# Performance work log

Hardware: AMD Instinct MI355X
Metric: run time of the kernel (lower is better)

Reference implementation:

```python
import jax, jax.numpy as jnp
import numpy as np
import math

N_USER = 100000
N_GAME = 50000
E = 200000
D = 256          # in_dim == out_dim
H = 8            # num_heads
SCALE = math.sqrt(D // H)  # sqrt(head_dim) = sqrt(32)


def setup_inputs() -> dict:
    key = jax.random.key(0)
    keys = jax.random.split(key, 64)
    it = iter(range(64))
    def nk():
        return keys[next(it)]
    s = 1.0 / math.sqrt(D)
    inp = {}
    inp["x_user"] = jax.random.normal(nk(), (N_USER, D), dtype=jnp.float32)
    inp["x_game"] = jax.random.normal(nk(), (N_GAME, D), dtype=jnp.float32)
    # node-type projections (k/q/v/out) for user and game
    for nt in ("user", "game"):
        for p in ("k", "q", "v", "out"):
            inp[f"W{p}_{nt}"] = jax.random.normal(nk(), (D, D), dtype=jnp.float32) * s
            inp[f"b{p}_{nt}"] = jax.random.normal(nk(), (D,), dtype=jnp.float32) * 0.01
    # edge-type attention + message transforms
    for et in ("played", "rev"):
        inp[f"Wa_{et}"] = jax.random.normal(nk(), (D, H), dtype=jnp.float32) * s
        inp[f"ba_{et}"] = jax.random.normal(nk(), (H,), dtype=jnp.float32) * 0.01
        inp[f"Wm_{et}"] = jax.random.normal(nk(), (D, D), dtype=jnp.float32) * s
        inp[f"bm_{et}"] = jax.random.normal(nk(), (D,), dtype=jnp.float32) * 0.01
    # edge indices: played (user -> game), rev_played (game -> user)
    inp["ei_played_src"] = jax.random.randint(nk(), (E,), 0, N_USER, dtype=jnp.int32)
    inp["ei_played_dst"] = jax.random.randint(nk(), (E,), 0, N_GAME, dtype=jnp.int32)
    inp["ei_rev_src"] = jax.random.randint(nk(), (E,), 0, N_GAME, dtype=jnp.int32)
    inp["ei_rev_dst"] = jax.random.randint(nk(), (E,), 0, N_USER, dtype=jnp.int32)
    return inp


def _lin(x, W, b):
    return x @ W + b


def _edge_pass(k_src_all, q_dst_all, v_src_all, Wa, ba, Wm, bm, src, dst, n_dst):
    # gather per-edge K/Q/V                                   [E, D]
    k_src = k_src_all[src]
    q_dst = q_dst_all[dst]
    v_src = v_src_all[src]
    # attention score MLP over head dim                       [E, H]
    scores = ((k_src * q_dst) @ Wa + ba) / SCALE
    attn = jax.nn.softmax(scores, axis=-1)  # softmax over heads (as in source)
    # message MLP                                             [E, D]
    msgs = v_src @ Wm + bm
    weighted = msgs * attn.mean(axis=-1, keepdims=True)
    # scatter-add to destination nodes
    agg = jax.ops.segment_sum(weighted, dst, num_segments=n_dst)
    cnt = jax.ops.segment_sum(jnp.ones((dst.shape[0], 1), weighted.dtype), dst, num_segments=n_dst)
    return agg, cnt


def reference(x_user, x_game,
              Wk_user, bk_user, Wq_user, bq_user, Wv_user, bv_user, Wout_user, bout_user,
              Wk_game, bk_game, Wq_game, bq_game, Wv_game, bv_game, Wout_game, bout_game,
              Wa_played, ba_played, Wm_played, bm_played,
              Wa_rev, ba_rev, Wm_rev, bm_rev,
              ei_played_src, ei_played_dst, ei_rev_src, ei_rev_dst):
    # per-node-type K/Q/V projections
    k_u = _lin(x_user, Wk_user, bk_user)
    q_u = _lin(x_user, Wq_user, bq_user)
    v_u = _lin(x_user, Wv_user, bv_user)
    k_g = _lin(x_game, Wk_game, bk_game)
    q_g = _lin(x_game, Wq_game, bq_game)
    v_g = _lin(x_game, Wv_game, bv_game)

    # user --played--> game
    agg_game, cnt_game = _edge_pass(k_u, q_g, v_u, Wa_played, ba_played, Wm_played, bm_played,
                                    ei_played_src, ei_played_dst, N_GAME)
    # game --rev_played--> user
    agg_user, cnt_user = _edge_pass(k_g, q_u, v_g, Wa_rev, ba_rev, Wm_rev, bm_rev,
                                    ei_rev_src, ei_rev_dst, N_USER)

    def finish(agg, cnt, x, Wout, bout):
        normed = agg / jnp.maximum(cnt, 1.0)
        return jax.nn.relu(_lin(normed, Wout, bout) + x)

    out_user = finish(agg_user, cnt_user, x_user, Wout_user, bout_user)
    out_game = finish(agg_game, cnt_game, x_game, Wout_game, bout_game)
    # concatenate node types for a single output array [N_USER+N_GAME, D]
    return jnp.concatenate([out_user, out_game], axis=0)
```

## Files before the change

kernel.cpp:

```cpp
#include <hip/hip_runtime.h>
#include <cstddef>


#define DD 256
#define SCAN_CHUNK 2048

typedef __attribute__((ext_vector_type(8))) short short8;
typedef __attribute__((ext_vector_type(4))) float floatx4;

__device__ __forceinline__ short f2bf(float f) {
    union { float f; unsigned u; } c;
    c.f = f;
    unsigned r = c.u + 0x7fffu + ((c.u >> 16) & 1u);
    return (short)(r >> 16);
}

__global__ __launch_bounds__(256) void fuseA(const float* __restrict__ A0,
                                             const float* __restrict__ B0,
                                             float* __restrict__ C0,
                                             const float* __restrict__ A1,
                                             const float* __restrict__ B1,
                                             float* __restrict__ C1,
                                             const int* __restrict__ dst0,
                                             int* __restrict__ cnt0, int E0,
                                             const int* __restrict__ dst1,
                                             int* __restrict__ cnt1, int E1) {
    __shared__ float As[DD];
    const int bid = blockIdx.x;
    const int c = threadIdx.x;
    if (bid < 512) {
        const int which = bid >> 8;
        const int r = bid & 255;
        const float* A = which ? A1 : A0;
        const float* B = which ? B1 : B0;
        float* C = which ? C1 : C0;
        As[c] = A[r * DD + c];
        __syncthreads();
        float acc = 0.f;
#pragma unroll 8
        for (int k = 0; k < DD; ++k) acc += As[k] * B[k * DD + c];
        C[r * DD + c] = acc;
    } else {
        const int nb0 = (E0 + 255) >> 8;
        const int b = bid - 512;
        if (b < nb0) {
            const int i = b * 256 + c;
            if (i < E0) atomicAdd(&cnt0[dst0[i]], 1);
        } else {
            const int i = (b - nb0) * 256 + c;
            if (i < E1) atomicAdd(&cnt1[dst1[i]], 1);
        }
    }
}

__global__ __launch_bounds__(256) void fuseB(const float* __restrict__ A0,
                                             const float* __restrict__ B0,
                                             short* __restrict__ C0,
                                             const float* __restrict__ A1,
                                             const float* __restrict__ B1,
                                             short* __restrict__ C1,
                                             int* __restrict__ off_g,
                                             int* __restrict__ sums_g, int n_g,
                                             int* __restrict__ off_u,
                                             int* __restrict__ sums_u, int n_u) {
    __shared__ float As[DD];
    __shared__ int ls[256];
    const int bid = blockIdx.x;
    const int tid = threadIdx.x;
    if (bid < 512) {
        const int which = bid >> 8;
        const int r = bid & 255;
        const int c = tid;
        const float* A = which ? A1 : A0;
        const float* B = which ? B1 : B0;
        short* C = which ? C1 : C0;
        As[c] = A[r * DD + c];
        __syncthreads();
        float acc = 0.f;
#pragma unroll 8
        for (int k = 0; k < DD; ++k) acc += As[k] * B[k * DD + c];
        const int idx = ((((r >> 5) * 16 + (c >> 4)) * 64 +
                          ((c & 15) | (((r >> 3) & 3) << 4))) << 3) + (r & 7);
        C[idx] = f2bf(acc * 0.125f);
    } else {
        const int nch_g = (n_g + SCAN_CHUNK - 1) / SCAN_CHUNK;
        const int b = bid - 512;
        int* off;
        int* sums;
        int n, cb;
        if (b < nch_g) { off = off_g; sums = sums_g; n = n_g; cb = b; }
        else { off = off_u; sums = sums_u; n = n_u; cb = b - nch_g; }
        const int base = cb * SCAN_CHUNK + tid * 8;
        int v[8];
        int s = 0;
#pragma unroll
        for (int i = 0; i < 8; ++i) {
            const int idx = base + i;
            v[i] = (idx < n) ? off[idx] : 0;
            s += v[i];
        }
        ls[tid] = s;
        __syncthreads();
        for (int d = 1; d < 256; d <<= 1) {
            const int t = (tid >= d) ? ls[tid - d] : 0;
            __syncthreads();
            ls[tid] += t;
            __syncthreads();
        }
        int excl = tid ? ls[tid - 1] : 0;
        if (tid == 255) sums[cb] = ls[255];
#pragma unroll
        for (int i = 0; i < 8; ++i) {
            const int idx = base + i;
            if (idx < n) off[idx] = excl;
            excl += v[i];
        }
    }
}

__global__ __launch_bounds__(256) void fuseC(const float* __restrict__ bv0,
                                             const float* __restrict__ Wm0,
                                             const float* __restrict__ bm0,
                                             const float* __restrict__ Wout0,
                                             float* __restrict__ bb0,
                                             const float* __restrict__ bv1,
                                             const float* __restrict__ Wm1,
                                             const float* __restrict__ bm1,
                                             const float* __restrict__ Wout1,
                                             float* __restrict__ bb1,
                                             int* __restrict__ sums_g, int nch_g,
                                             int* __restrict__ sums_u, int nch_u) {
    __shared__ float t[DD];
    __shared__ int ls[256];
    const int tid = threadIdx.x;
    if (blockIdx.x < 2) {
        const int w = blockIdx.x;
        const float* bv = w ? bv1 : bv0;
        const float* Wm = w ? Wm1 : Wm0;
        const float* bm = w ? bm1 : bm0;
        const float* Wout = w ? Wout1 : Wout0;
        float* bb = w ? bb1 : bb0;
        float acc = bm[tid];
#pragma unroll 8
        for (int k = 0; k < DD; ++k) acc += bv[k] * Wm[k * DD + tid];
        t[tid] = acc;
        __syncthreads();
        float acc2 = 0.f;
#pragma unroll 8
        for (int k = 0; k < DD; ++k) acc2 += t[k] * Wout[k * DD + tid];
        bb[tid] = acc2 * 0.125f;
    } else {
        int* sums = (blockIdx.x == 2) ? sums_g : sums_u;
        const int nch = (blockIdx.x == 2) ? nch_g : nch_u;
        ls[tid] = (tid < nch) ? sums[tid] : 0;
        __syncthreads();
        for (int d = 1; d < 256; d <<= 1) {
            const int t2 = (tid >= d) ? ls[tid - d] : 0;
            __syncthreads();
            ls[tid] += t2;
            __syncthreads();
        }
        if (tid < nch) sums[tid] = tid ? ls[tid - 1] : 0;
    }
}

__global__ __launch_bounds__(256) void fuseD(int* __restrict__ off_g,
                                             const int* __restrict__ sums_g,
                                             int* __restrict__ cur_g, int n_g, int Eg,
                                             int* __restrict__ off_u,
                                             const int* __restrict__ sums_u,
                                             int* __restrict__ cur_u, int n_u, int Eu) {
    const int gidx = blockIdx.x * 256 + threadIdx.x;
    const int span_g = n_g + 1;
    if (gidx < span_g) {
        if (gidx < n_g) {
            const int v = off_g[gidx] + sums_g[gidx / SCAN_CHUNK];
            off_g[gidx] = v;
            cur_g[gidx] = v;
        } else {
            off_g[n_g] = Eg;
        }
    } else {
        const int idx = gidx - span_g;
        if (idx < n_u) {
            const int v = off_u[idx] + sums_u[idx / SCAN_CHUNK];
            off_u[idx] = v;
            cur_u[idx] = v;
        } else if (idx == n_u) {
            off_u[n_u] = Eu;
        }
    }
}

__global__ __launch_bounds__(256) void fuseE(const int* __restrict__ src0,
                                             const int* __restrict__ dst0,
                                             int* __restrict__ cur0,
                                             int* __restrict__ perm0, int E0,
                                             const int* __restrict__ src1,
                                             const int* __restrict__ dst1,
                                             int* __restrict__ cur1,
                                             int* __restrict__ perm1, int E1) {
    const int nb0 = (E0 + 255) >> 8;
    const int b = blockIdx.x;
    const int tid = threadIdx.x;
    if (b < nb0) {
        const int i = b * 256 + tid;
        if (i < E0) {
            const int pos = atomicAdd(&cur0[dst0[i]], 1);
            perm0[pos] = src0[i];
        }
    } else {
        const int i = (b - nb0) * 256 + tid;
        if (i < E1) {
            const int pos = atomicAdd(&cur1[dst1[i]], 1);
            perm1[pos] = src1[i];
        }
    }
}

__global__ __launch_bounds__(256, 4) void agg_gemm2(
    const float* __restrict__ x_user, const float* __restrict__ x_game,
    const int* __restrict__ perm_rev, const int* __restrict__ off_user,
    const short* __restrict__ Bsw_rev, const float* __restrict__ bb_rev,
    const float* __restrict__ bout_user,
    const int* __restrict__ perm_played, const int* __restrict__ off_game,
    const short* __restrict__ Bsw_played, const float* __restrict__ bb_played,
    const float* __restrict__ bout_game,
    float* __restrict__ outp, int n_user, int n_game, int nb_game) {
    __shared__ short As[32][264];
    __shared__ float bt[32];

    const int tid = threadIdx.x;
    const int wave = __builtin_amdgcn_readfirstlane(tid >> 6);
    const int lane = tid & 63;

    const float* x_src;
    const float* x_res;
    const int* perm;
    const int* off;
    const short* Bsw;
    const float* bb;
    const float* bout;
    float* out;
    int M, r0;
    if ((int)blockIdx.x < nb_game) {
        x_src = x_user; x_res = x_game;
        perm = perm_played; off = off_game;
        Bsw = Bsw_played; bb = bb_played; bout = bout_game;
        out = outp + (size_t)n_user * DD;
        M = n_game;
        r0 = (int)blockIdx.x * 32;
    } else {
        x_src = x_game; x_res = x_user;
        perm = perm_rev; off = off_user;
        Bsw = Bsw_rev; bb = bb_rev; bout = bout_user;
        out = outp;
        M = n_user;
        r0 = ((int)blockIdx.x - nb_game) * 32;
    }

    int e[8], en[8], deg[8];
    float4 acc[8];
#pragma unroll
    for (int j = 0; j < 8; ++j) {
        const int r = r0 + wave * 8 + j;
        e[j] = (r < M) ? off[r] : 0;
        en[j] = (r < M) ? off[r + 1] : 0;
        deg[j] = en[j] - e[j];
        acc[j].x = 0.f; acc[j].y = 0.f; acc[j].z = 0.f; acc[j].w = 0.f;
    }
    int mdeg = 0;
#pragma unroll
    for (int j = 0; j < 8; ++j) mdeg = max(mdeg, deg[j]);
    for (int t = 0; t < mdeg; ++t) {
        float4 v[8];
        bool h[8];
#pragma unroll
        for (int j = 0; j < 8; ++j) {
            h[j] = e[j] < en[j];
            if (h[j]) {
                const int s = perm[e[j]++];
                v[j] = ((const float4*)(x_src + (size_t)s * DD))[lane];
            }
        }
#pragma unroll
        for (int j = 0; j < 8; ++j) {
            if (h[j]) {
                acc[j].x += v[j].x;
                acc[j].y += v[j].y;
                acc[j].z += v[j].z;
                acc[j].w += v[j].w;
            }
        }
    }
#pragma unroll
    for (int j = 0; j < 8; ++j) {
        const int lr = wave * 8 + j;
        const float inv = 1.0f / fmaxf((float)deg[j], 1.0f);
        short4 b4;
        b4.x = f2bf(acc[j].x * inv);
        b4.y = f2bf(acc[j].y * inv);
        b4.z = f2bf(acc[j].z * inv);
        b4.w = f2bf(acc[j].w * inv);
        *(short4*)&As[lr][lane * 4] = b4;
        if (lane == 0) bt[lr] = (deg[j] > 0) ? 1.0f : 0.0f;
    }
    __syncthreads();

    const int quad = lane >> 4;
    const int l16 = lane & 15;
    floatx4 cacc[2][4];
#pragma unroll
    for (int rt = 0; rt < 2; ++rt)
#pragma unroll
        for (int ct = 0; ct < 4; ++ct) cacc[rt][ct] = (floatx4){0.f, 0.f, 0.f, 0.f};

    for (int kb8 = 0; kb8 < 8; ++kb8) {
        short8 af[2];
#pragma unroll
        for (int rt = 0; rt < 2; ++rt)
            af[rt] = *(const short8*)&As[rt * 16 + l16][kb8 * 32 + quad * 8];
        short8 bf[4];
        const short* bp = Bsw + (((size_t)(kb8 * 16 + wave * 4) * 64 + lane) << 3);
#pragma unroll
        for (int ct = 0; ct < 4; ++ct)
            bf[ct] = *(const short8*)(bp + (ct << 9));
#pragma unroll
        for (int rt = 0; rt < 2; ++rt)
#pragma unroll
            for (int ct = 0; ct < 4; ++ct)
                cacc[rt][ct] = __builtin_amdgcn_mfma_f32_16x16x32_bf16(
                    af[rt], bf[ct], cacc[rt][ct], 0, 0, 0);
    }

    float bbv[4], bov[4];
#pragma unroll
    for (int ct = 0; ct < 4; ++ct) {
        const int n = wave * 64 + ct * 16 + l16;
        bbv[ct] = bb[n];
        bov[ct] = bout[n];
    }
#pragma unroll
    for (int rt = 0; rt < 2; ++rt) {
#pragma unroll
        for (int j = 0; j < 4; ++j) {
            const int lr = rt * 16 + quad * 4 + j;
            const int r = r0 + lr;
            if (r < M) {
                const float btv = bt[lr];
                const float* xr = x_res + (size_t)r * DD;
                float* orow = out + (size_t)r * DD;
#pragma unroll
                for (int ct = 0; ct < 4; ++ct) {
                    const int n = wave * 64 + ct * 16 + l16;
                    const float o = cacc[rt][ct][j] + btv * bbv[ct] + bov[ct] + xr[n];
                    orow[n] = fmaxf(o, 0.f);
                }
            }
        }
    }
}

extern "C" void kernel_launch(void* const* d_in, const int* in_sizes, int n_in,
                              void* d_out, int out_size, void* d_ws, size_t ws_size,
                              hipStream_t stream) {
    const float* x_user = (const float*)d_in[0];
    const float* x_game = (const float*)d_in[1];
    const float* Wv_user = (const float*)d_in[6];
    const float* bv_user = (const float*)d_in[7];
    const float* Wout_user = (const float*)d_in[8];
    const float* bout_user = (const float*)d_in[9];
    const float* Wv_game = (const float*)d_in[14];
    const float* bv_game = (const float*)d_in[15];
    const float* Wout_game = (const float*)d_in[16];
    const float* bout_game = (const float*)d_in[17];
    const float* Wm_played = (const float*)d_in[20];
    const float* bm_played = (const float*)d_in[21];
    const float* Wm_rev = (const float*)d_in[24];
    const float* bm_rev = (const float*)d_in[25];
    const int* ei_played_src = (const int*)d_in[26];
    const int* ei_played_dst = (const int*)d_in[27];
    const int* ei_rev_src = (const int*)d_in[28];
    const int* ei_rev_dst = (const int*)d_in[29];

    const int n_user = in_sizes[0] / DD;
    const int n_game = in_sizes[1] / DD;
    const int e_played = in_sizes[26];
    const int e_rev = in_sizes[28];

    float* out = (float*)d_out;

    float* fws = (float*)d_ws;
    float* T0 = fws;
    float* T1 = T0 + DD * DD;
    float* bb_played = T1 + DD * DD;
    float* bb_rev = bb_played + DD;
    short* Bsw_played = (short*)(bb_rev + DD);
    short* Bsw_rev = Bsw_played + DD * DD;
    int* iws = (int*)(Bsw_rev + DD * DD);
    int* off_game = iws;
    int* off_user = off_game + (n_game + 1);
    int* cursor_game = off_user + (n_user + 1);
    int* cursor_user = cursor_game + n_game;
    int* sums_game = cursor_user + n_user;
    int* sums_user = sums_game + 256;
    int* perm_played = sums_user + 256;
    int* perm_rev = perm_played + e_played;
    (void)ws_size; (void)n_in; (void)out_size;

    hipMemsetAsync(off_game, 0, (size_t)(n_game + n_user + 2) * sizeof(int), stream);

    const int nbh_p = (e_played + 255) / 256;
    const int nbh_r = (e_rev + 255) / 256;
    const int nch_g = (n_game + SCAN_CHUNK - 1) / SCAN_CHUNK;
    const int nch_u = (n_user + SCAN_CHUNK - 1) / SCAN_CHUNK;

    fuseA<<<512 + nbh_p + nbh_r, 256, 0, stream>>>(
        Wv_user, Wm_played, T0, Wv_game, Wm_rev, T1,
        ei_played_dst, off_game, e_played, ei_rev_dst, off_user, e_rev);
    fuseB<<<512 + nch_g + nch_u, 256, 0, stream>>>(
        T0, Wout_game, Bsw_played, T1, Wout_user, Bsw_rev,
        off_game, sums_game, n_game, off_user, sums_user, n_user);
    fuseC<<<4, 256, 0, stream>>>(
        bv_user, Wm_played, bm_played, Wout_game, bb_played,
        bv_game, Wm_rev, bm_rev, Wout_user, bb_rev,
        sums_game, nch_g, sums_user, nch_u);
    const int ntot = (n_game + 1) + (n_user + 1);
    fuseD<<<(ntot + 255) / 256, 256, 0, stream>>>(
        off_game, sums_game, cursor_game, n_game, e_played,
        off_user, sums_user, cursor_user, n_user, e_rev);
    fuseE<<<nbh_p + nbh_r, 256, 0, stream>>>(
        ei_played_src, ei_played_dst, cursor_game, perm_played, e_played,
        ei_rev_src, ei_rev_dst, cursor_user, perm_rev, e_rev);

    const int nb_game = (n_game + 31) / 32;
    const int nb_user = (n_user + 31) / 32;
    agg_gemm2<<<nb_game + nb_user, 256, 0, stream>>>(
        x_user, x_game, perm_rev, off_user, Bsw_rev, bb_rev, bout_user,
        perm_played, off_game, Bsw_played, bb_played, bout_game,
        out, n_user, n_game, nb_game);
}
```

Measured before the change: 473.1 us.

## Project source nodes before aggregation and gather bf16 rows instead of fp32

The folded (Wv·Wm·Wout) GEMM now runs per source node before the scatter-mean, producing bf16 projected rows Y, and that GEMM is merged into the CSR-fill kernel. The final kernel then gathers half-width bf16 rows, averages them and applies bias, residual and ReLU with no GEMM. This halves the bytes read in the gather-heavy aggregation and removes the MFMA work from the final pass. In exchange it adds a dense GEMM over all 150k source nodes plus a bf16 write and read of Y, and rounds each row to bf16 before summation, which adds some numerical error.

```diff
diff --git a/kernel.cpp b/kernel.cpp
--- a/kernel.cpp
+++ b/kernel.cpp
@@ -1,5 +1,6 @@
 #include <hip/hip_runtime.h>
 #include <cstddef>
+#include <cstdint>
 
 
 #define DD 256
@@ -13,6 +14,17 @@
     c.f = f;
     unsigned r = c.u + 0x7fffu + ((c.u >> 16) & 1u);
     return (short)(r >> 16);
+}
+
+__device__ __forceinline__ float bflo(unsigned u) {
+    union { unsigned u; float f; } c;
+    c.u = u << 16;
+    return c.f;
+}
+__device__ __forceinline__ float bfhi(unsigned u) {
+    union { unsigned u; float f; } c;
+    c.u = u & 0xffff0000u;
+    return c.f;
 }
 
 __global__ __launch_bounds__(256) void fuseA(const float* __restrict__ A0,
@@ -192,68 +204,146 @@
     }
 }
 
-__global__ __launch_bounds__(256) void fuseE(const int* __restrict__ src0,
-                                             const int* __restrict__ dst0,
-                                             int* __restrict__ cur0,
-                                             int* __restrict__ perm0, int E0,
-                                             const int* __restrict__ src1,
-                                             const int* __restrict__ dst1,
-                                             int* __restrict__ cur1,
-                                             int* __restrict__ perm1, int E1) {
-    const int nb0 = (E0 + 255) >> 8;
-    const int b = blockIdx.x;
+__global__ __launch_bounds__(256, 4) void fuseE(
+    const int* __restrict__ src0, const int* __restrict__ dst0,
+    int* __restrict__ cur0, int* __restrict__ perm0, int E0,
+    const int* __restrict__ src1, const int* __restrict__ dst1,
+    int* __restrict__ cur1, int* __restrict__ perm1, int E1,
+    const float* __restrict__ x_user, const float* __restrict__ x_game,
+    const short* __restrict__ Bswp, const short* __restrict__ Bswr,
+    short* __restrict__ Yp, short* __restrict__ Yr,
+    int n_user, int n_game, int nyb_u, int nyb_g) {
+    __shared__ short As[32][264];
+    const int bid = blockIdx.x;
     const int tid = threadIdx.x;
-    if (b < nb0) {
-        const int i = b * 256 + tid;
-        if (i < E0) {
-            const int pos = atomicAdd(&cur0[dst0[i]], 1);
-            perm0[pos] = src0[i];
-        }
-    } else {
-        const int i = (b - nb0) * 256 + tid;
-        if (i < E1) {
-            const int pos = atomicAdd(&cur1[dst1[i]], 1);
-            perm1[pos] = src1[i];
-        }
-    }
-}
-
-__global__ __launch_bounds__(256, 4) void agg_gemm2(
+    const int nyb = nyb_u + nyb_g;
+    if (bid < nyb) {
+        const int wave = __builtin_amdgcn_readfirstlane(tid >> 6);
+        const int lane = tid & 63;
+        const float* X;
+        short* Y;
+        const short* Bsw;
+        int M, r0;
+        if (bid < nyb_u) { X = x_user; Y = Yp; Bsw = Bswp; M = n_user; r0 = bid * 32; }
+        else { X = x_game; Y = Yr; Bsw = Bswr; M = n_game; r0 = (bid - nyb_u) * 32; }
+
+#pragma unroll
+        for (int j = 0; j < 8; ++j) {
+            const int lr = wave * 8 + j;
+            const int r = r0 + lr;
+            short4 b4 = {0, 0, 0, 0};
+            if (r < M) {
+                const float4 v = ((const float4*)(X + (size_t)r * DD))[lane];
+                b4.x = f2bf(v.x);
+                b4.y = f2bf(v.y);
+                b4.z = f2bf(v.z);
+                b4.w = f2bf(v.w);
+            }
+            *(short4*)&As[lr][lane * 4] = b4;
+        }
+        __syncthreads();
+
+        const int quad = lane >> 4;
+        const int l16 = lane & 15;
+        floatx4 cacc[2][4];
+#pragma unroll
+        for (int rt = 0; rt < 2; ++rt)
+#pragma unroll
+            for (int ct = 0; ct < 4; ++ct) cacc[rt][ct] = (floatx4){0.f, 0.f, 0.f, 0.f};
+
+        for (int kb8 = 0; kb8 < 8; ++kb8) {
+            short8 af[2];
+#pragma unroll
+            for (int rt = 0; rt < 2; ++rt)
+                af[rt] = *(const short8*)&As[rt * 16 + l16][kb8 * 32 + quad * 8];
+            short8 bf[4];
+            const short* bp = Bsw + (((size_t)(kb8 * 16 + wave * 4) * 64 + lane) << 3);
+#pragma unroll
+            for (int ct = 0; ct < 4; ++ct)
+                bf[ct] = *(const short8*)(bp + (ct << 9));
+#pragma unroll
+            for (int rt = 0; rt < 2; ++rt)
+#pragma unroll
+                for (int ct = 0; ct < 4; ++ct)
+                    cacc[rt][ct] = __builtin_amdgcn_mfma_f32_16x16x32_bf16(
+                        af[rt], bf[ct], cacc[rt][ct], 0, 0, 0);
+        }
+        __syncthreads();
+
+#pragma unroll
+        for (int rt = 0; rt < 2; ++rt)
+#pragma unroll
+            for (int ct = 0; ct < 4; ++ct)
+#pragma unroll
+                for (int j = 0; j < 4; ++j)
+                    As[rt * 16 + quad * 4 + j][wave * 64 + ct * 16 + l16] =
+                        f2bf(cacc[rt][ct][j]);
+        __syncthreads();
+#pragma unroll
+        for (int j = 0; j < 8; ++j) {
+            const int lr = wave * 8 + j;
+            const int r = r0 + lr;
+            if (r < M)
+                *(short4*)(Y + (size_t)r * DD + lane * 4) =
+                    *(const short4*)&As[lr][lane * 4];
+        }
+    } else {
+        const int b = bid - nyb;
+        const int nb0 = (E0 + 255) >> 8;
+        if (b < nb0) {
+            const int i = b * 256 + tid;
+            if (i < E0) {
+                const int pos = atomicAdd(&cur0[dst0[i]], 1);
+                perm0[pos] = src0[i];
+            }
+        } else {
+            const int i = (b - nb0) * 256 + tid;
+            if (i < E1) {
+                const int pos = atomicAdd(&cur1[dst1[i]], 1);
+                perm1[pos] = src1[i];
+            }
+        }
+    }
+}
+
+__global__ __launch_bounds__(256, 4) void agg_relu(
+    const short* __restrict__ Yp, const short* __restrict__ Yr,
+    const int* __restrict__ perm_rev, const int* __restrict__ off_user,
+    const float* __restrict__ bb_rev, const float* __restrict__ bout_user,
+    const int* __restrict__ perm_played, const int* __restrict__ off_game,
+    const float* __restrict__ bb_played, const float* __restrict__ bout_game,
     const float* __restrict__ x_user, const float* __restrict__ x_game,
-    const int* __restrict__ perm_rev, const int* __restrict__ off_user,
-    const short* __restrict__ Bsw_rev, const float* __restrict__ bb_rev,
-    const float* __restrict__ bout_user,
-    const int* __restrict__ perm_played, const int* __restrict__ off_game,
-    const short* __restrict__ Bsw_played, const float* __restrict__ bb_played,
-    const float* __restrict__ bout_game,
     float* __restrict__ outp, int n_user, int n_game, int nb_game) {
-    __shared__ short As[32][264];
-    __shared__ float bt[32];
-
     const int tid = threadIdx.x;
     const int wave = __builtin_amdgcn_readfirstlane(tid >> 6);
     const int lane = tid & 63;
-
-    const float* x_src;
-    const float* x_res;
+    const int n0 = lane * 4;
+
+    const short* Y;
     const int* perm;
     const int* off;
-    const short* Bsw;
     const float* bb;
     const float* bout;
+    const float* x_res;
     float* out;
     int M, r0;
     if ((int)blockIdx.x < nb_game) {
-        x_src = x_user; x_res = x_game;
-        perm = perm_played; off = off_game;
-        Bsw = Bsw_played; bb = bb_played; bout = bout_game;
+        Y = Yp;
+        perm = perm_played;
+        off = off_game;
+        bb = bb_played;
+        bout = bout_game;
+        x_res = x_game;
         out = outp + (size_t)n_user * DD;
         M = n_game;
         r0 = (int)blockIdx.x * 32;
     } else {
-        x_src = x_game; x_res = x_user;
-        perm = perm_rev; off = off_user;
-        Bsw = Bsw_rev; bb = bb_rev; bout = bout_user;
+        Y = Yr;
+        perm = perm_rev;
+        off = off_user;
+        bb = bb_rev;
+        bout = bout_user;
+        x_res = x_user;
         out = outp;
         M = n_user;
         r0 = ((int)blockIdx.x - nb_game) * 32;
@@ -267,96 +357,52 @@
         e[j] = (r < M) ? off[r] : 0;
         en[j] = (r < M) ? off[r + 1] : 0;
         deg[j] = en[j] - e[j];
-        acc[j].x = 0.f; acc[j].y = 0.f; acc[j].z = 0.f; acc[j].w = 0.f;
+        acc[j].x = 0.f;
+        acc[j].y = 0.f;
+        acc[j].z = 0.f;
+        acc[j].w = 0.f;
     }
     int mdeg = 0;
 #pragma unroll
     for (int j = 0; j < 8; ++j) mdeg = max(mdeg, deg[j]);
+
     for (int t = 0; t < mdeg; ++t) {
-        float4 v[8];
+        uint2 d[8];
         bool h[8];
 #pragma unroll
         for (int j = 0; j < 8; ++j) {
             h[j] = e[j] < en[j];
             if (h[j]) {
                 const int s = perm[e[j]++];
-                v[j] = ((const float4*)(x_src + (size_t)s * DD))[lane];
+                d[j] = *(const uint2*)(Y + (size_t)s * DD + n0);
             }
         }
 #pragma unroll
         for (int j = 0; j < 8; ++j) {
             if (h[j]) {
-                acc[j].x += v[j].x;
-                acc[j].y += v[j].y;
-                acc[j].z += v[j].z;
-                acc[j].w += v[j].w;
+                acc[j].x += bflo(d[j].x);
+                acc[j].y += bfhi(d[j].x);
+                acc[j].z += bflo(d[j].y);
+                acc[j].w += bfhi(d[j].y);
             }
         }
     }
+
+    const float4 bbv = *(const float4*)(bb + n0);
+    const float4 bov = *(const float4*)(bout + n0);
 #pragma unroll
     for (int j = 0; j < 8; ++j) {
-        const int lr = wave * 8 + j;
-        const float inv = 1.0f / fmaxf((float)deg[j], 1.0f);
-        short4 b4;
-        b4.x = f2bf(acc[j].x * inv);
-        b4.y = f2bf(acc[j].y * inv);
-        b4.z = f2bf(acc[j].z * inv);
-        b4.w = f2bf(acc[j].w * inv);
-        *(short4*)&As[lr][lane * 4] = b4;
-        if (lane == 0) bt[lr] = (deg[j] > 0) ? 1.0f : 0.0f;
-    }
-    __syncthreads();
-
-    const int quad = lane >> 4;
-    const int l16 = lane & 15;
-    floatx4 cacc[2][4];
-#pragma unroll
-    for (int rt = 0; rt < 2; ++rt)
-#pragma unroll
-        for (int ct = 0; ct < 4; ++ct) cacc[rt][ct] = (floatx4){0.f, 0.f, 0.f, 0.f};
-
-    for (int kb8 = 0; kb8 < 8; ++kb8) {
-        short8 af[2];
-#pragma unroll
-        for (int rt = 0; rt < 2; ++rt)
-            af[rt] = *(const short8*)&As[rt * 16 + l16][kb8 * 32 + quad * 8];
-        short8 bf[4];
-        const short* bp = Bsw + (((size_t)(kb8 * 16 + wave * 4) * 64 + lane) << 3);
-#pragma unroll
-        for (int ct = 0; ct < 4; ++ct)
-            bf[ct] = *(const short8*)(bp + (ct << 9));
-#pragma unroll
-        for (int rt = 0; rt < 2; ++rt)
-#pragma unroll
-            for (int ct = 0; ct < 4; ++ct)
-                cacc[rt][ct] = __builtin_amdgcn_mfma_f32_16x16x32_bf16(
-                    af[rt], bf[ct], cacc[rt][ct], 0, 0, 0);
-    }
-
-    float bbv[4], bov[4];
-#pragma unroll
-    for (int ct = 0; ct < 4; ++ct) {
-        const int n = wave * 64 + ct * 16 + l16;
-        bbv[ct] = bb[n];
-        bov[ct] = bout[n];
-    }
-#pragma unroll
-    for (int rt = 0; rt < 2; ++rt) {
-#pragma unroll
-        for (int j = 0; j < 4; ++j) {
-            const int lr = rt * 16 + quad * 4 + j;
-            const int r = r0 + lr;
-            if (r < M) {
-                const float btv = bt[lr];
-                const float* xr = x_res + (size_t)r * DD;
-                float* orow = out + (size_t)r * DD;
-#pragma unroll
-                for (int ct = 0; ct < 4; ++ct) {
-                    const int n = wave * 64 + ct * 16 + l16;
-                    const float o = cacc[rt][ct][j] + btv * bbv[ct] + bov[ct] + xr[n];
-                    orow[n] = fmaxf(o, 0.f);
-                }
-            }
+        const int r = r0 + wave * 8 + j;
+        if (r < M) {
+            const float inv = 1.0f / fmaxf((float)deg[j], 1.0f);
+            const float beta = (deg[j] > 0) ? 1.0f : 0.0f;
+            const float4 xr = *(const float4*)(x_res + (size_t)r * DD + n0);
+            float4 o;
+            o.x = fmaxf(acc[j].x * inv + beta * bbv.x + bov.x + xr.x, 0.f);
+            o.y = fmaxf(acc[j].y * inv + beta * bbv.y + bov.y + xr.y, 0.f);
+            o.z = fmaxf(acc[j].z * inv + beta * bbv.z + bov.z + xr.z, 0.f);
+            o.w = fmaxf(acc[j].w * inv + beta * bbv.w + bov.w + xr.w, 0.f);
+            *(float4*)(out + (size_t)r * DD + n0) = o;
         }
     }
 }
@@ -406,6 +452,10 @@
     int* sums_user = sums_game + 256;
     int* perm_played = sums_user + 256;
     int* perm_rev = perm_played + e_played;
+    uintptr_t yaddr = (uintptr_t)(perm_rev + e_rev);
+    yaddr = (yaddr + 255) & ~(uintptr_t)255;
+    short* Yp = (short*)yaddr;
+    short* Yr = Yp + (size_t)n_user * DD;
     (void)ws_size; (void)n_in; (void)out_size;
 
     hipMemsetAsync(off_game, 0, (size_t)(n_game + n_user + 2) * sizeof(int), stream);
@@ -429,14 +479,18 @@
     fuseD<<<(ntot + 255) / 256, 256, 0, stream>>>(
         off_game, sums_game, cursor_game, n_game, e_played,
         off_user, sums_user, cursor_user, n_user, e_rev);
-    fuseE<<<nbh_p + nbh_r, 256, 0, stream>>>(
+    const int nyb_u = (n_user + 31) / 32;
+    const int nyb_g = (n_game + 31) / 32;
+    fuseE<<<nyb_u + nyb_g + nbh_p + nbh_r, 256, 0, stream>>>(
         ei_played_src, ei_played_dst, cursor_game, perm_played, e_played,
-        ei_rev_src, ei_rev_dst, cursor_user, perm_rev, e_rev);
+        ei_rev_src, ei_rev_dst, cursor_user, perm_rev, e_rev,
+        x_user, x_game, Bsw_played, Bsw_rev, Yp, Yr,
+        n_user, n_game, nyb_u, nyb_g);
 
     const int nb_game = (n_game + 31) / 32;
     const int nb_user = (n_user + 31) / 32;
-    agg_gemm2<<<nb_game + nb_user, 256, 0, stream>>>(
-        x_user, x_game, perm_rev, off_user, Bsw_rev, bb_rev, bout_user,
-        perm_played, off_game, Bsw_played, bb_played, bout_game,
-        out, n_user, n_game, nb_game);
-}
+    agg_relu<<<nb_game + nb_user, 256, 0, stream>>>(
+        Yp, Yr, perm_rev, off_user, bb_rev, bout_user,
+        perm_played, off_game, bb_played, bout_game,
+        x_user, x_game, out, n_user, n_game, nb_game);
+}
```

New measurement: 486.6 us. 2.9% more time.

## Sort destination rows by in-degree to balance per-wave aggregation work

Applied to the files above, without the earlier changes.

Computes a per-node degree histogram during the scan, builds a degree-sorted row permutation (descending, capped at 63) via counting sort, and has the aggregation GEMM kernel process rows in that order. Rows in a wave and block then have similar degrees, so the gather loop bound (max degree among 8 rows) wastes fewer iterations. In exchange it adds extra passes and atomics in the prep kernels, plus indirection for residual and output rows, which makes those reads and writes scattered rather than contiguous.

```diff
diff --git a/kernel.cpp b/kernel.cpp
--- a/kernel.cpp
+++ b/kernel.cpp
@@ -1,5 +1,6 @@
 #include <hip/hip_runtime.h>
 #include <cstddef>
+#include <cstdint>
 
 
 #define DD 256
@@ -62,9 +63,12 @@
                                              int* __restrict__ off_g,
                                              int* __restrict__ sums_g, int n_g,
                                              int* __restrict__ off_u,
-                                             int* __restrict__ sums_u, int n_u) {
+                                             int* __restrict__ sums_u, int n_u,
+                                             unsigned char* __restrict__ deg8,
+                                             int* __restrict__ dbin) {
     __shared__ float As[DD];
     __shared__ int ls[256];
+    __shared__ int lhist[64];
     const int bid = blockIdx.x;
     const int tid = threadIdx.x;
     if (bid < 512) {
@@ -87,9 +91,14 @@
         const int b = bid - 512;
         int* off;
         int* sums;
-        int n, cb;
-        if (b < nch_g) { off = off_g; sums = sums_g; n = n_g; cb = b; }
-        else { off = off_u; sums = sums_u; n = n_u; cb = b - nch_g; }
+        int n, cb, degbase, dbbase;
+        if (b < nch_g) {
+            off = off_g; sums = sums_g; n = n_g; cb = b; degbase = 0; dbbase = 0;
+        } else {
+            off = off_u; sums = sums_u; n = n_u; cb = b - nch_g;
+            degbase = n_g; dbbase = 64;
+        }
+        if (tid < 64) lhist[tid] = 0;
         const int base = cb * SCAN_CHUNK + tid * 8;
         int v[8];
         int s = 0;
@@ -101,6 +110,16 @@
         }
         ls[tid] = s;
         __syncthreads();
+#pragma unroll
+        for (int i = 0; i < 8; ++i) {
+            const int idx = base + i;
+            if (idx < n) {
+                const int d = v[i];
+                deg8[degbase + idx] = (unsigned char)(d > 255 ? 255 : d);
+                const int bin = 63 - (d > 63 ? 63 : d);
+                atomicAdd(&lhist[bin], 1);
+            }
+        }
         for (int d = 1; d < 256; d <<= 1) {
             const int t = (tid >= d) ? ls[tid - d] : 0;
             __syncthreads();
@@ -115,6 +134,8 @@
             if (idx < n) off[idx] = excl;
             excl += v[i];
         }
+        __syncthreads();
+        if (tid < 64 && lhist[tid]) atomicAdd(&dbin[dbbase + tid], lhist[tid]);
     }
 }
 
@@ -129,7 +150,9 @@
                                              const float* __restrict__ Wout1,
                                              float* __restrict__ bb1,
                                              int* __restrict__ sums_g, int nch_g,
-                                             int* __restrict__ sums_u, int nch_u) {
+                                             int* __restrict__ sums_u, int nch_u,
+                                             const int* __restrict__ dbin,
+                                             int* __restrict__ dcur) {
     __shared__ float t[DD];
     __shared__ int ls[256];
     const int tid = threadIdx.x;
@@ -149,7 +172,7 @@
 #pragma unroll 8
         for (int k = 0; k < DD; ++k) acc2 += t[k] * Wout[k * DD + tid];
         bb[tid] = acc2 * 0.125f;
-    } else {
+    } else if (blockIdx.x < 4) {
         int* sums = (blockIdx.x == 2) ? sums_g : sums_u;
         const int nch = (blockIdx.x == 2) ? nch_g : nch_u;
         ls[tid] = (tid < nch) ? sums[tid] : 0;
@@ -161,6 +184,16 @@
             __syncthreads();
         }
         if (tid < nch) sums[tid] = tid ? ls[tid - 1] : 0;
+    } else {
+        ls[tid] = (tid < 128) ? dbin[tid] : 0;
+        __syncthreads();
+        for (int d = 1; d < 64; d <<= 1) {
+            const int t2 = ((tid & 63) >= d) ? ls[tid - d] : 0;
+            __syncthreads();
+            ls[tid] += t2;
+            __syncthreads();
+        }
+        if (tid < 128) dcur[tid] = (tid & 63) ? ls[tid - 1] : 0;
     }
 }
 
@@ -169,14 +202,28 @@
                                              int* __restrict__ cur_g, int n_g, int Eg,
                                              int* __restrict__ off_u,
                                              const int* __restrict__ sums_u,
-                                             int* __restrict__ cur_u, int n_u, int Eu) {
-    const int gidx = blockIdx.x * 256 + threadIdx.x;
+                                             int* __restrict__ cur_u, int n_u, int Eu,
+                                             const unsigned char* __restrict__ deg8,
+                                             int* __restrict__ dcur,
+                                             int* __restrict__ rowperm_g,
+                                             int* __restrict__ rowperm_u) {
+    __shared__ int lh[128];
+    __shared__ int lb[128];
+    const int tid = threadIdx.x;
+    const int gidx = blockIdx.x * 256 + tid;
     const int span_g = n_g + 1;
+    if (tid < 128) lh[tid] = 0;
+    __syncthreads();
+
+    int bin = -1, rowid = -1, rank = 0;
     if (gidx < span_g) {
         if (gidx < n_g) {
             const int v = off_g[gidx] + sums_g[gidx / SCAN_CHUNK];
             off_g[gidx] = v;
             cur_g[gidx] = v;
+            const int d = deg8[gidx];
+            bin = 63 - (d > 63 ? 63 : d);
+            rowid = gidx;
         } else {
             off_g[n_g] = Eg;
         }
@@ -186,9 +233,21 @@
             const int v = off_u[idx] + sums_u[idx / SCAN_CHUNK];
             off_u[idx] = v;
             cur_u[idx] = v;
+            const int d = deg8[n_g + idx];
+            bin = 64 + 63 - (d > 63 ? 63 : d);
+            rowid = idx;
         } else if (idx == n_u) {
             off_u[n_u] = Eu;
         }
+    }
+    if (bin >= 0) rank = atomicAdd(&lh[bin], 1);
+    __syncthreads();
+    if (tid < 128 && lh[tid]) lb[tid] = atomicAdd(&dcur[tid], lh[tid]);
+    __syncthreads();
+    if (bin >= 0) {
+        const int pos = lb[bin] + rank;
+        if (bin < 64) rowperm_g[pos] = rowid;
+        else rowperm_u[pos] = rowid;
     }
 }
 
@@ -218,17 +277,18 @@
     }
 }
 
-__global__ __launch_bounds__(256, 4) void agg_gemm2(
+__global__ __launch_bounds__(256, 4) void agg_gemm4(
     const float* __restrict__ x_user, const float* __restrict__ x_game,
     const int* __restrict__ perm_rev, const int* __restrict__ off_user,
     const short* __restrict__ Bsw_rev, const float* __restrict__ bb_rev,
-    const float* __restrict__ bout_user,
+    const float* __restrict__ bout_user, const int* __restrict__ rowperm_u,
     const int* __restrict__ perm_played, const int* __restrict__ off_game,
     const short* __restrict__ Bsw_played, const float* __restrict__ bb_played,
-    const float* __restrict__ bout_game,
+    const float* __restrict__ bout_game, const int* __restrict__ rowperm_g,
     float* __restrict__ outp, int n_user, int n_game, int nb_game) {
     __shared__ short As[32][264];
     __shared__ float bt[32];
+    __shared__ int rsh[32];
 
     const int tid = threadIdx.x;
     const int wave = __builtin_amdgcn_readfirstlane(tid >> 6);
@@ -241,12 +301,14 @@
     const short* Bsw;
     const float* bb;
     const float* bout;
+    const int* rperm;
     float* out;
     int M, r0;
     if ((int)blockIdx.x < nb_game) {
         x_src = x_user; x_res = x_game;
         perm = perm_played; off = off_game;
         Bsw = Bsw_played; bb = bb_played; bout = bout_game;
+        rperm = rowperm_g;
         out = outp + (size_t)n_user * DD;
         M = n_game;
         r0 = (int)blockIdx.x * 32;
@@ -254,6 +316,7 @@
         x_src = x_game; x_res = x_user;
         perm = perm_rev; off = off_user;
         Bsw = Bsw_rev; bb = bb_rev; bout = bout_user;
+        rperm = rowperm_u;
         out = outp;
         M = n_user;
         r0 = ((int)blockIdx.x - nb_game) * 32;
@@ -263,15 +326,22 @@
     float4 acc[8];
 #pragma unroll
     for (int j = 0; j < 8; ++j) {
-        const int r = r0 + wave * 8 + j;
-        e[j] = (r < M) ? off[r] : 0;
-        en[j] = (r < M) ? off[r + 1] : 0;
+        const int slot = r0 + wave * 8 + j;
+        const int rs = (slot < M) ? rperm[slot] : -1;
+        e[j] = (rs >= 0) ? off[rs] : 0;
+        en[j] = (rs >= 0) ? off[rs + 1] : 0;
         deg[j] = en[j] - e[j];
         acc[j].x = 0.f; acc[j].y = 0.f; acc[j].z = 0.f; acc[j].w = 0.f;
+        if (lane == 0) {
+            const int lr = wave * 8 + j;
+            rsh[lr] = rs;
+            bt[lr] = (deg[j] > 0) ? 1.0f : 0.0f;
+        }
     }
     int mdeg = 0;
 #pragma unroll
     for (int j = 0; j < 8; ++j) mdeg = max(mdeg, deg[j]);
+
     for (int t = 0; t < mdeg; ++t) {
         float4 v[8];
         bool h[8];
@@ -303,7 +373,6 @@
         b4.z = f2bf(acc[j].z * inv);
         b4.w = f2bf(acc[j].w * inv);
         *(short4*)&As[lr][lane * 4] = b4;
-        if (lane == 0) bt[lr] = (deg[j] > 0) ? 1.0f : 0.0f;
     }
     __syncthreads();
 
@@ -345,11 +414,11 @@
 #pragma unroll
         for (int j = 0; j < 4; ++j) {
             const int lr = rt * 16 + quad * 4 + j;
-            const int r = r0 + lr;
-            if (r < M) {
+            if (r0 + lr < M) {
+                const int rs = rsh[lr];
                 const float btv = bt[lr];
-                const float* xr = x_res + (size_t)r * DD;
-                float* orow = out + (size_t)r * DD;
+                const float* xr = x_res + (size_t)rs * DD;
+                float* orow = out + (size_t)rs * DD;
 #pragma unroll
                 for (int ct = 0; ct < 4; ++ct) {
                     const int n = wave * 64 + ct * 16 + l16;
@@ -398,17 +467,23 @@
     short* Bsw_played = (short*)(bb_rev + DD);
     short* Bsw_rev = Bsw_played + DD * DD;
     int* iws = (int*)(Bsw_rev + DD * DD);
-    int* off_game = iws;
+    int* dbin = iws;
+    int* off_game = dbin + 128;
     int* off_user = off_game + (n_game + 1);
-    int* cursor_game = off_user + (n_user + 1);
+    int* dcur = off_user + (n_user + 1);
+    int* cursor_game = dcur + 128;
     int* cursor_user = cursor_game + n_game;
     int* sums_game = cursor_user + n_user;
     int* sums_user = sums_game + 256;
     int* perm_played = sums_user + 256;
     int* perm_rev = perm_played + e_played;
+    int* rowperm_g = perm_rev + e_rev;
+    int* rowperm_u = rowperm_g + n_game;
+    unsigned char* deg8 = (unsigned char*)(rowperm_u + n_user);
     (void)ws_size; (void)n_in; (void)out_size;
 
-    hipMemsetAsync(off_game, 0, (size_t)(n_game + n_user + 2) * sizeof(int), stream);
+    hipMemsetAsync(dbin, 0, (size_t)(128 + (n_game + 1) + (n_user + 1)) * sizeof(int),
+                   stream);
 
     const int nbh_p = (e_played + 255) / 256;
     const int nbh_r = (e_rev + 255) / 256;
@@ -420,23 +495,25 @@
         ei_played_dst, off_game, e_played, ei_rev_dst, off_user, e_rev);
     fuseB<<<512 + nch_g + nch_u, 256, 0, stream>>>(
         T0, Wout_game, Bsw_played, T1, Wout_user, Bsw_rev,
-        off_game, sums_game, n_game, off_user, sums_user, n_user);
-    fuseC<<<4, 256, 0, stream>>>(
+        off_game, sums_game, n_game, off_user, sums_user, n_user,
+        deg8, dbin);
+    fuseC<<<5, 256, 0, stream>>>(
         bv_user, Wm_played, bm_played, Wout_game, bb_played,
         bv_game, Wm_rev, bm_rev, Wout_user, bb_rev,
-        sums_game, nch_g, sums_user, nch_u);
+        sums_game, nch_g, sums_user, nch_u, dbin, dcur);
     const int ntot = (n_game + 1) + (n_user + 1);
     fuseD<<<(ntot + 255) / 256, 256, 0, stream>>>(
         off_game, sums_game, cursor_game, n_game, e_played,
-        off_user, sums_user, cursor_user, n_user, e_rev);
+        off_user, sums_user, cursor_user, n_user, e_rev,
+        deg8, dcur, rowperm_g, rowperm_u);
     fuseE<<<nbh_p + nbh_r, 256, 0, stream>>>(
         ei_played_src, ei_played_dst, cursor_game, perm_played, e_played,
         ei_rev_src, ei_rev_dst, cursor_user, perm_rev, e_rev);
 
     const int nb_game = (n_game + 31) / 32;
     const int nb_user = (n_user + 31) / 32;
-    agg_gemm2<<<nb_game + nb_user, 256, 0, stream>>>(
-        x_user, x_game, perm_rev, off_user, Bsw_rev, bb_rev, bout_user,
-        perm_played, off_game, Bsw_played, bb_played, bout_game,
+    agg_gemm4<<<nb_game + nb_user, 256, 0, stream>>>(
+        x_user, x_game, perm_rev, off_user, Bsw_rev, bb_rev, bout_user, rowperm_u,
+        perm_played, off_game, Bsw_played, bb_played, bout_game, rowperm_g,
         out, n_user, n_game, nb_game);
 }
```

Result: slower. 484.0 us (+2.3%).
